# Kernel tuning notes

Hardware: AMD Instinct MI355X
Metric: run time of the kernel (lower is better)

The kernel has to match this reference:

```python
import jax, jax.numpy as jnp
import numpy as np

B, P, D = 16384, 4096, 256

def setup_inputs() -> dict:
    key = jax.random.key(0)
    kx, kp = jax.random.split(key)
    x = jax.random.normal(kx, (B, D), dtype=jnp.float32)
    prototypes = jax.random.normal(kp, (P, D), dtype=jnp.float32)
    return {"x": x, "prototypes": prototypes}

def reference(x, prototypes):
    # Pairwise L2 distance: ||x - p||_2 for every (batch, prototype) pair.
    # GEMM reformulation avoids the O(B*P*D) broadcast intermediate:
    x_sq = jnp.sum(x * x, axis=-1, keepdims=True)                 # [B, 1]
    p_sq = jnp.sum(prototypes * prototypes, axis=-1)[None, :]     # [1, P]
    xp = jnp.einsum('bd,pd->bp', x, prototypes)                   # [B, P]
    sq_dist = jnp.maximum(x_sq + p_sq - 2.0 * xp, 0.0)
    return jnp.sqrt(sq_dist)                                      # [B, P]
```

## Files before the change

### kernel.cpp

```cpp
#include <hip/hip_runtime.h>
#include <hip/hip_bf16.h>

#define B_DIM 16384
#define P_DIM 4096
#define D_DIM 256

typedef float f32x4 __attribute__((ext_vector_type(4)));
typedef __bf16 bf16x8 __attribute__((ext_vector_type(8)));

__device__ __forceinline__ unsigned short f2bf_rne(float f) {
  unsigned int u = __builtin_bit_cast(unsigned int, f);
  u += 0x7fffu + ((u >> 16) & 1u);
  return (unsigned short)(u >> 16);
}

__global__ __launch_bounds__(256) void prep_kernel(
    const float* __restrict__ x, const float* __restrict__ p,
    unsigned short* __restrict__ xb, unsigned short* __restrict__ pb,
    float* __restrict__ xsq, float* __restrict__ psq) {
  int row  = blockIdx.x * 4 + (threadIdx.x >> 6);
  int lane = threadIdx.x & 63;
  const float4* src;
  unsigned short* dst;
  float* sq;
  if (row < B_DIM) {
    src = (const float4*)(x + (size_t)row * D_DIM);
    dst = xb + (size_t)row * D_DIM;
    sq  = xsq + row;
  } else {
    int r = row - B_DIM;
    src = (const float4*)(p + (size_t)r * D_DIM);
    dst = pb + (size_t)r * D_DIM;
    sq  = psq + r;
  }
  float4 v = src[lane];
  ushort4 o;
  o.x = f2bf_rne(v.x); o.y = f2bf_rne(v.y);
  o.z = f2bf_rne(v.z); o.w = f2bf_rne(v.w);
  ((ushort4*)dst)[lane] = o;
  float s = v.x * v.x + v.y * v.y + v.z * v.z + v.w * v.w;
  #pragma unroll
  for (int off = 32; off > 0; off >>= 1) s += __shfl_down(s, off);
  if (lane == 0) *sq = s;
}

__device__ __forceinline__ void async16(const unsigned short* g, void* l) {
  __builtin_amdgcn_global_load_lds(
      (const __attribute__((address_space(1))) void*)g,
      (__attribute__((address_space(3))) void*)l,
      16, 0, 0);
}

__global__ __launch_bounds__(256, 2) void dist_gemm(
    const unsigned short* __restrict__ A,
    const unsigned short* __restrict__ Bm,
    const float* __restrict__ xsq, const float* __restrict__ psq,
    float* __restrict__ out) {
  __shared__ __align__(16) __bf16 As[128 * 32];
  __shared__ __align__(16) __bf16 Bs[128 * 32];

  const int tid  = threadIdx.x;
  const int w    = tid >> 6;
  const int lane = tid & 63;

  const int bid = blockIdx.x;
  const int swz = (bid & 7) * 512 + (bid >> 3);
  const int bm  = swz >> 5;
  const int bn  = swz & 31;

  const int wr = w >> 1;
  const int wc = w & 1;

  f32x4 acc[4][4];
  #pragma unroll
  for (int m = 0; m < 4; ++m)
    #pragma unroll
    for (int n = 0; n < 4; ++n) acc[m][n] = 0.0f;

  const int ofs0 = w * 2048 + lane * 16;
  const int ofs1 = ofs0 + 1024;
  const int r0 = ofs0 >> 6, c0 = (ofs0 & 63) >> 1;
  const int r1 = ofs1 >> 6, c1 = (ofs1 & 63) >> 1;

  const unsigned short* a0 = A  + (size_t)(bm * 128 + r0) * D_DIM + c0;
  const unsigned short* a1 = A  + (size_t)(bm * 128 + r1) * D_DIM + c1;
  const unsigned short* b0 = Bm + (size_t)(bn * 128 + r0) * D_DIM + c0;
  const unsigned short* b1 = Bm + (size_t)(bn * 128 + r1) * D_DIM + c1;

  char* ldsA = (char*)As + w * 2048;
  char* ldsB = (char*)Bs + w * 2048;

  const int ar = wr * 64 + (lane & 15);
  const int br = wc * 64 + (lane & 15);
  const int kk = (lane >> 4) * 8;

  #pragma unroll 1
  for (int kt = 0; kt < D_DIM; kt += 32) {
    async16(a0 + kt, ldsA);
    async16(a1 + kt, ldsA + 1024);
    async16(b0 + kt, ldsB);
    async16(b1 + kt, ldsB + 1024);
    __syncthreads();

    bf16x8 av[4], bv[4];
    #pragma unroll
    for (int m = 0; m < 4; ++m)
      av[m] = *(const bf16x8*)(As + (ar + m * 16) * 32 + kk);
    #pragma unroll
    for (int n = 0; n < 4; ++n)
      bv[n] = *(const bf16x8*)(Bs + (br + n * 16) * 32 + kk);

    #pragma unroll
    for (int m = 0; m < 4; ++m)
      #pragma unroll
      for (int n = 0; n < 4; ++n)
        acc[m][n] = __builtin_amdgcn_mfma_f32_16x16x32_bf16(av[m], bv[n], acc[m][n], 0, 0, 0);
    __syncthreads();
  }

  const int row0 = bm * 128 + wr * 64 + (lane >> 4) * 4;
  const int col0 = bn * 128 + wc * 64 + (lane & 15);
  #pragma unroll
  for (int m = 0; m < 4; ++m) {
    #pragma unroll
    for (int n = 0; n < 4; ++n) {
      const int col = col0 + n * 16;
      const float ps = psq[col];
      #pragma unroll
      for (int j = 0; j < 4; ++j) {
        const int row = row0 + m * 16 + j;
        const float xs = xsq[row];
        float v = fmaf(-2.0f, acc[m][n][j], xs + ps);
        v = fmaxf(v, 0.0f);
        out[(size_t)row * P_DIM + col] = __builtin_sqrtf(v);
      }
    }
  }
}

extern "C" void kernel_launch(void* const* d_in, const int* in_sizes, int n_in,
                              void* d_out, int out_size, void* d_ws, size_t ws_size,
                              hipStream_t stream) {
  const float* x = (const float*)d_in[0];
  const float* p = (const float*)d_in[1];
  float* out = (float*)d_out;

  char* ws = (char*)d_ws;
  unsigned short* xb = (unsigned short*)ws;
  unsigned short* pb = (unsigned short*)(ws + (size_t)B_DIM * D_DIM * 2);
  float* xsq = (float*)(ws + (size_t)(B_DIM + P_DIM) * D_DIM * 2);
  float* psq = xsq + B_DIM;

  prep_kernel<<<(B_DIM + P_DIM) / 4, 256, 0, stream>>>(x, p, xb, pb, xsq, psq);

  dist_gemm<<<(B_DIM / 128) * (P_DIM / 128), 256, 0, stream>>>(xb, pb, xsq, psq, out);
}
```

Measured before the change: 89.35 us.

## Double-buffer LDS with BK=64, XOR-swizzled layout and nontemporal output stores

Raises the K tile from 32 to 64 and double-buffers the LDS tiles, so the async global-to-LDS loads for the next tile overlap the MFMA work on the current one and each tile needs only one barrier. The LDS layout gets an XOR swizzle on the row index to cut bank conflicts on the bf16x8 fragment reads. Output stores become nontemporal to avoid polluting the cache with the large result. LDS use grows to 64KB per block, which may limit occupancy against the launch-bounds target of 2 blocks per CU.

```diff
diff --git a/kernel.cpp b/kernel.cpp
--- a/kernel.cpp
+++ b/kernel.cpp
@@ -4,6 +4,8 @@
 #define B_DIM 16384
 #define P_DIM 4096
 #define D_DIM 256
+#define BK 64
+#define NT (D_DIM / BK)
 
 typedef float f32x4 __attribute__((ext_vector_type(4)));
 typedef __bf16 bf16x8 __attribute__((ext_vector_type(8)));
@@ -56,8 +58,7 @@
     const unsigned short* __restrict__ Bm,
     const float* __restrict__ xsq, const float* __restrict__ psq,
     float* __restrict__ out) {
-  __shared__ __align__(16) __bf16 As[128 * 32];
-  __shared__ __align__(16) __bf16 Bs[128 * 32];
+  __shared__ __align__(16) char lds[2][2][128 * BK * 2];
 
   const int tid  = threadIdx.x;
   const int w    = tid >> 6;
@@ -77,45 +78,67 @@
     #pragma unroll
     for (int n = 0; n < 4; ++n) acc[m][n] = 0.0f;
 
-  const int ofs0 = w * 2048 + lane * 16;
-  const int ofs1 = ofs0 + 1024;
-  const int r0 = ofs0 >> 6, c0 = (ofs0 & 63) >> 1;
-  const int r1 = ofs1 >> 6, c1 = (ofs1 & 63) >> 1;
+  const unsigned short* asrc[4];
+  const unsigned short* bsrc[4];
+  int lofs[4];
+  #pragma unroll
+  for (int l = 0; l < 4; ++l) {
+    int q  = w * 4096 + l * 1024 + lane * 16;
+    int r  = q >> 7;
+    int cb = (q & 127) ^ ((r & 7) << 4);
+    asrc[l] = A  + (size_t)(bm * 128 + r) * D_DIM + (cb >> 1);
+    bsrc[l] = Bm + (size_t)(bn * 128 + r) * D_DIM + (cb >> 1);
+    lofs[l] = w * 4096 + l * 1024;
+  }
 
-  const unsigned short* a0 = A  + (size_t)(bm * 128 + r0) * D_DIM + c0;
-  const unsigned short* a1 = A  + (size_t)(bm * 128 + r1) * D_DIM + c1;
-  const unsigned short* b0 = Bm + (size_t)(bn * 128 + r0) * D_DIM + c0;
-  const unsigned short* b1 = Bm + (size_t)(bn * 128 + r1) * D_DIM + c1;
+#define STAGE(buf, kt) do {                                      \
+    _Pragma("unroll")                                            \
+    for (int l = 0; l < 4; ++l) {                                \
+      async16(asrc[l] + (kt), (void*)(lds[buf][0] + lofs[l]));   \
+      async16(bsrc[l] + (kt), (void*)(lds[buf][1] + lofs[l]));   \
+    } } while (0)
 
-  char* ldsA = (char*)As + w * 2048;
-  char* ldsB = (char*)Bs + w * 2048;
+  const int ar   = wr * 64 + (lane & 15);
+  const int br   = wc * 64 + (lane & 15);
+  const int xr   = (lane & 7) << 4;
+  const int kcol = (lane >> 4) * 16;
 
-  const int ar = wr * 64 + (lane & 15);
-  const int br = wc * 64 + (lane & 15);
-  const int kk = (lane >> 4) * 8;
+  STAGE(0, 0);
+  asm volatile("s_waitcnt vmcnt(0)" ::: "memory");
+  __builtin_amdgcn_s_barrier();
+  __builtin_amdgcn_sched_barrier(0);
 
-  #pragma unroll 1
-  for (int kt = 0; kt < D_DIM; kt += 32) {
-    async16(a0 + kt, ldsA);
-    async16(a1 + kt, ldsA + 1024);
-    async16(b0 + kt, ldsB);
-    async16(b1 + kt, ldsB + 1024);
-    __syncthreads();
+  #pragma unroll
+  for (int t = 0; t < NT; ++t) {
+    if (t < NT - 1) STAGE((t + 1) & 1, (t + 1) * BK);
 
-    bf16x8 av[4], bv[4];
+    const char* La = lds[t & 1][0];
+    const char* Lb = lds[t & 1][1];
     #pragma unroll
-    for (int m = 0; m < 4; ++m)
-      av[m] = *(const bf16x8*)(As + (ar + m * 16) * 32 + kk);
-    #pragma unroll
-    for (int n = 0; n < 4; ++n)
-      bv[n] = *(const bf16x8*)(Bs + (br + n * 16) * 32 + kk);
+    for (int qk = 0; qk < 2; ++qk) {
+      bf16x8 av[4], bv[4];
+      #pragma unroll
+      for (int m = 0; m < 4; ++m) {
+        int row = ar + m * 16;
+        av[m] = *(const bf16x8*)(La + row * 128 + ((kcol + qk * 64) ^ xr));
+      }
+      #pragma unroll
+      for (int n = 0; n < 4; ++n) {
+        int row = br + n * 16;
+        bv[n] = *(const bf16x8*)(Lb + row * 128 + ((kcol + qk * 64) ^ xr));
+      }
+      #pragma unroll
+      for (int m = 0; m < 4; ++m)
+        #pragma unroll
+        for (int n = 0; n < 4; ++n)
+          acc[m][n] = __builtin_amdgcn_mfma_f32_16x16x32_bf16(av[m], bv[n], acc[m][n], 0, 0, 0);
+    }
 
-    #pragma unroll
-    for (int m = 0; m < 4; ++m)
-      #pragma unroll
-      for (int n = 0; n < 4; ++n)
-        acc[m][n] = __builtin_amdgcn_mfma_f32_16x16x32_bf16(av[m], bv[n], acc[m][n], 0, 0, 0);
-    __syncthreads();
+    if (t < NT - 1) {
+      asm volatile("s_waitcnt vmcnt(0)" ::: "memory");
+      __builtin_amdgcn_s_barrier();
+      __builtin_amdgcn_sched_barrier(0);
+    }
   }
 
   const int row0 = bm * 128 + wr * 64 + (lane >> 4) * 4;
@@ -132,10 +155,12 @@
         const float xs = xsq[row];
         float v = fmaf(-2.0f, acc[m][n][j], xs + ps);
         v = fmaxf(v, 0.0f);
-        out[(size_t)row * P_DIM + col] = __builtin_sqrtf(v);
+        __builtin_nontemporal_store(__builtin_sqrtf(v),
+                                    &out[(size_t)row * P_DIM + col]);
       }
     }
   }
+#undef STAGE
 }
 
 extern "C" void kernel_launch(void* const* d_in, const int* in_sizes, int n_in,
```

Result: slower. 92.72 us (+3.8%).

## Pre-swizzle bf16 operands into MFMA fragment layout and drop LDS staging

Applied to the files above, without the earlier changes.

The prep kernel now writes x and prototypes in bf16 using a blocked layout that matches the MFMA 16x16x32 fragment order. The GEMM can then have each wave load its operand fragments straight from global memory with coalesced 16-byte loads, which removes the LDS copies and the __syncthreads barriers. The block tiling changes to a 64-row A tile shared by four waves, each covering a different 64-column group. The launch bound rises to 3 blocks per CU, and the grid is mapped by XCD so neighbouring blocks reuse A in L2. The cost is that the four waves do not share their B fragments, so there is no reuse through LDS and more data comes from L2.

```diff
diff --git a/kernel.cpp b/kernel.cpp
--- a/kernel.cpp
+++ b/kernel.cpp
@@ -18,58 +18,61 @@
     const float* __restrict__ x, const float* __restrict__ p,
     unsigned short* __restrict__ xb, unsigned short* __restrict__ pb,
     float* __restrict__ xsq, float* __restrict__ psq) {
-  int row  = blockIdx.x * 4 + (threadIdx.x >> 6);
-  int lane = threadIdx.x & 63;
-  const float4* src;
+  const int rg = blockIdx.x;
+  const int t = threadIdx.x;
+  const int row = t >> 4;
+  const int kq  = t & 15;
+
+  const float* src;
   unsigned short* dst;
   float* sq;
-  if (row < B_DIM) {
-    src = (const float4*)(x + (size_t)row * D_DIM);
-    dst = xb + (size_t)row * D_DIM;
-    sq  = xsq + row;
+  if (rg < B_DIM / 16) {
+    src = x + (size_t)rg * 16 * D_DIM;
+    dst = xb + (size_t)rg * 4096;
+    sq  = xsq + rg * 16;
   } else {
-    int r = row - B_DIM;
-    src = (const float4*)(p + (size_t)r * D_DIM);
-    dst = pb + (size_t)r * D_DIM;
-    sq  = psq + r;
+    const int r = rg - B_DIM / 16;
+    src = p + (size_t)r * 16 * D_DIM;
+    dst = pb + (size_t)r * 4096;
+    sq  = psq + r * 16;
   }
-  float4 v = src[lane];
-  ushort4 o;
-  o.x = f2bf_rne(v.x); o.y = f2bf_rne(v.y);
-  o.z = f2bf_rne(v.z); o.w = f2bf_rne(v.w);
-  ((ushort4*)dst)[lane] = o;
-  float s = v.x * v.x + v.y * v.y + v.z * v.z + v.w * v.w;
+
+  float s = 0.0f;
   #pragma unroll
-  for (int off = 32; off > 0; off >>= 1) s += __shfl_down(s, off);
-  if (lane == 0) *sq = s;
+  for (int pass = 0; pass < 4; ++pass) {
+    float4 v = *(const float4*)(src + row * D_DIM + pass * 64 + kq * 4);
+    s += v.x * v.x + v.y * v.y + v.z * v.z + v.w * v.w;
+    ushort4 o;
+    o.x = f2bf_rne(v.x); o.y = f2bf_rne(v.y);
+    o.z = f2bf_rne(v.z); o.w = f2bf_rne(v.w);
+    const int kc = pass * 8 + (kq >> 1);
+    *(ushort4*)(dst + kc * 128 + row * 8 + (kq & 1) * 4) = o;
+  }
+  s += __shfl_xor(s, 1);
+  s += __shfl_xor(s, 2);
+  s += __shfl_xor(s, 4);
+  s += __shfl_xor(s, 8);
+  if (kq == 0) sq[row] = s;
 }
 
-__device__ __forceinline__ void async16(const unsigned short* g, void* l) {
-  __builtin_amdgcn_global_load_lds(
-      (const __attribute__((address_space(1))) void*)g,
-      (__attribute__((address_space(3))) void*)l,
-      16, 0, 0);
-}
-
-__global__ __launch_bounds__(256, 2) void dist_gemm(
-    const unsigned short* __restrict__ A,
-    const unsigned short* __restrict__ Bm,
+__global__ __launch_bounds__(256, 3) void dist_gemm(
+    const unsigned short* __restrict__ A2,
+    const unsigned short* __restrict__ B2,
     const float* __restrict__ xsq, const float* __restrict__ psq,
     float* __restrict__ out) {
-  __shared__ __align__(16) __bf16 As[128 * 32];
-  __shared__ __align__(16) __bf16 Bs[128 * 32];
-
   const int tid  = threadIdx.x;
   const int w    = tid >> 6;
   const int lane = tid & 63;
+  const int bid  = blockIdx.x;
 
-  const int bid = blockIdx.x;
-  const int swz = (bid & 7) * 512 + (bid >> 3);
-  const int bm  = swz >> 5;
-  const int bn  = swz & 31;
+  const int xcd = bid & 7;
+  const int idx = bid >> 3;
+  const int am  = idx >> 1;
+  const int bnb = xcd * 2 + (idx & 1);
+  const int bn  = bnb * 4 + w;
 
-  const int wr = w >> 1;
-  const int wc = w & 1;
+  const char* Abase = (const char*)A2 + (size_t)am * 32768 + lane * 16;
+  const char* Bbase = (const char*)B2 + (size_t)bn * 32768 + lane * 16;
 
   f32x4 acc[4][4];
   #pragma unroll
@@ -77,62 +80,41 @@
     #pragma unroll
     for (int n = 0; n < 4; ++n) acc[m][n] = 0.0f;
 
-  const int ofs0 = w * 2048 + lane * 16;
-  const int ofs1 = ofs0 + 1024;
-  const int r0 = ofs0 >> 6, c0 = (ofs0 & 63) >> 1;
-  const int r1 = ofs1 >> 6, c1 = (ofs1 & 63) >> 1;
-
-  const unsigned short* a0 = A  + (size_t)(bm * 128 + r0) * D_DIM + c0;
-  const unsigned short* a1 = A  + (size_t)(bm * 128 + r1) * D_DIM + c1;
-  const unsigned short* b0 = Bm + (size_t)(bn * 128 + r0) * D_DIM + c0;
-  const unsigned short* b1 = Bm + (size_t)(bn * 128 + r1) * D_DIM + c1;
-
-  char* ldsA = (char*)As + w * 2048;
-  char* ldsB = (char*)Bs + w * 2048;
-
-  const int ar = wr * 64 + (lane & 15);
-  const int br = wc * 64 + (lane & 15);
-  const int kk = (lane >> 4) * 8;
-
-  #pragma unroll 1
-  for (int kt = 0; kt < D_DIM; kt += 32) {
-    async16(a0 + kt, ldsA);
-    async16(a1 + kt, ldsA + 1024);
-    async16(b0 + kt, ldsB);
-    async16(b1 + kt, ldsB + 1024);
-    __syncthreads();
-
+  #pragma unroll
+  for (int kt = 0; kt < 8; ++kt) {
     bf16x8 av[4], bv[4];
     #pragma unroll
     for (int m = 0; m < 4; ++m)
-      av[m] = *(const bf16x8*)(As + (ar + m * 16) * 32 + kk);
+      av[m] = *(const bf16x8*)(Abase + m * 8192 + kt * 1024);
     #pragma unroll
     for (int n = 0; n < 4; ++n)
-      bv[n] = *(const bf16x8*)(Bs + (br + n * 16) * 32 + kk);
-
+      bv[n] = *(const bf16x8*)(Bbase + n * 8192 + kt * 1024);
     #pragma unroll
     for (int m = 0; m < 4; ++m)
       #pragma unroll
       for (int n = 0; n < 4; ++n)
         acc[m][n] = __builtin_amdgcn_mfma_f32_16x16x32_bf16(av[m], bv[n], acc[m][n], 0, 0, 0);
-    __syncthreads();
   }
 
-  const int row0 = bm * 128 + wr * 64 + (lane >> 4) * 4;
-  const int col0 = bn * 128 + wc * 64 + (lane & 15);
+  const int rowb = am * 64 + ((lane >> 4) << 2);
+  const int colb = bn * 64 + (lane & 15);
+  f32x4 xs4[4];
+  #pragma unroll
+  for (int m = 0; m < 4; ++m)
+    xs4[m] = *(const f32x4*)(xsq + rowb + m * 16);
+  float psv[4];
+  #pragma unroll
+  for (int n = 0; n < 4; ++n) psv[n] = psq[colb + n * 16];
+
   #pragma unroll
   for (int m = 0; m < 4; ++m) {
     #pragma unroll
-    for (int n = 0; n < 4; ++n) {
-      const int col = col0 + n * 16;
-      const float ps = psq[col];
+    for (int j = 0; j < 4; ++j) {
+      float* orow = out + (size_t)(rowb + m * 16 + j) * P_DIM + colb;
       #pragma unroll
-      for (int j = 0; j < 4; ++j) {
-        const int row = row0 + m * 16 + j;
-        const float xs = xsq[row];
-        float v = fmaf(-2.0f, acc[m][n][j], xs + ps);
-        v = fmaxf(v, 0.0f);
-        out[(size_t)row * P_DIM + col] = __builtin_sqrtf(v);
+      for (int n = 0; n < 4; ++n) {
+        float v = fmaf(-2.0f, acc[m][n][j], xs4[m][j] + psv[n]);
+        orow[n * 16] = __builtin_sqrtf(fmaxf(v, 0.0f));
       }
     }
   }
@@ -151,7 +133,7 @@
   float* xsq = (float*)(ws + (size_t)(B_DIM + P_DIM) * D_DIM * 2);
   float* psq = xsq + B_DIM;
 
-  prep_kernel<<<(B_DIM + P_DIM) / 4, 256, 0, stream>>>(x, p, xb, pb, xsq, psq);
+  prep_kernel<<<(B_DIM + P_DIM) / 16, 256, 0, stream>>>(x, p, xb, pb, xsq, psq);
 
-  dist_gemm<<<(B_DIM / 128) * (P_DIM / 128), 256, 0, stream>>>(xb, pb, xsq, psq, out);
+  dist_gemm<<<4096, 256, 0, stream>>>(xb, pb, xsq, psq, out);
 }
```

New measurement: 104.5 us. 17.0% more time.

## Triple-buffer LDS pipeline with swizzled layout and vectorized epilogue stores

Applied to the files above, without the earlier changes.

Replaces the single-buffer load/sync/compute loop with a three-stage LDS ring fed by async global-to-LDS loads, using vmcnt waits and one barrier per step so the next tiles' loads overlap the MFMA work. The LDS layout is XOR-swizzled to reduce bank conflicts on fragment reads, and the MFMA operands are swapped so each lane holds four consecutive output columns. That lets the epilogue write float4 stores, cutting store instruction count, and raises the occupancy hint to 3 blocks per CU. The cost is more LDS per block and hand-tuned waitcnt logic that depends on how the compiler schedules the loads.

```diff
diff --git a/kernel.cpp b/kernel.cpp
--- a/kernel.cpp
+++ b/kernel.cpp
@@ -4,6 +4,8 @@
 #define B_DIM 16384
 #define P_DIM 4096
 #define D_DIM 256
+#define BK 32
+#define NSTEP (D_DIM / BK)
 
 typedef float f32x4 __attribute__((ext_vector_type(4)));
 typedef __bf16 bf16x8 __attribute__((ext_vector_type(8)));
@@ -44,26 +46,25 @@
   if (lane == 0) *sq = s;
 }
 
-__device__ __forceinline__ void async16(const unsigned short* g, void* l) {
+__device__ __forceinline__ void async16(const unsigned short* g, const void* l) {
   __builtin_amdgcn_global_load_lds(
       (const __attribute__((address_space(1))) void*)g,
       (__attribute__((address_space(3))) void*)l,
       16, 0, 0);
 }
 
-__global__ __launch_bounds__(256, 2) void dist_gemm(
+__global__ __launch_bounds__(256, 3) void dist_gemm(
     const unsigned short* __restrict__ A,
     const unsigned short* __restrict__ Bm,
     const float* __restrict__ xsq, const float* __restrict__ psq,
     float* __restrict__ out) {
-  __shared__ __align__(16) __bf16 As[128 * 32];
-  __shared__ __align__(16) __bf16 Bs[128 * 32];
+  __shared__ __align__(16) char lds[3][2][8192];
 
   const int tid  = threadIdx.x;
   const int w    = tid >> 6;
   const int lane = tid & 63;
+  const int bid  = blockIdx.x;
 
-  const int bid = blockIdx.x;
   const int swz = (bid & 7) * 512 + (bid >> 3);
   const int bm  = swz >> 5;
   const int bn  = swz & 31;
@@ -71,71 +72,87 @@
   const int wr = w >> 1;
   const int wc = w & 1;
 
+  const int trow = tid >> 2;
+  const int tcol = (((tid & 3) ^ (trow & 3)) << 3);
+  const unsigned short* aSrc = A  + (size_t)(bm * 128 + trow) * D_DIM + tcol;
+  const unsigned short* bSrc = Bm + (size_t)(bn * 128 + trow) * D_DIM + tcol;
+  const int ldst = tid * 16;
+
+#define STAGE(bufi, ktE) do { _Pragma("unroll")                                \
+    for (int i = 0; i < 2; ++i) {                                              \
+      async16(aSrc + (size_t)i * 64 * D_DIM + (ktE),                           \
+              (const void*)(&lds[bufi][0][0] + i * 4096 + ldst));              \
+      async16(bSrc + (size_t)i * 64 * D_DIM + (ktE),                           \
+              (const void*)(&lds[bufi][1][0] + i * 4096 + ldst));              \
+    } } while (0)
+
+  const int arow = wr * 64 + (lane & 15);
+  const int brow = wc * 64 + (lane & 15);
+  const int koff = (((lane >> 4) ^ (lane & 3)) << 4);
+
   f32x4 acc[4][4];
   #pragma unroll
   for (int m = 0; m < 4; ++m)
     #pragma unroll
     for (int n = 0; n < 4; ++n) acc[m][n] = 0.0f;
 
-  const int ofs0 = w * 2048 + lane * 16;
-  const int ofs1 = ofs0 + 1024;
-  const int r0 = ofs0 >> 6, c0 = (ofs0 & 63) >> 1;
-  const int r1 = ofs1 >> 6, c1 = (ofs1 & 63) >> 1;
+  STAGE(0, 0);
+  STAGE(1, BK);
 
-  const unsigned short* a0 = A  + (size_t)(bm * 128 + r0) * D_DIM + c0;
-  const unsigned short* a1 = A  + (size_t)(bm * 128 + r1) * D_DIM + c1;
-  const unsigned short* b0 = Bm + (size_t)(bn * 128 + r0) * D_DIM + c0;
-  const unsigned short* b1 = Bm + (size_t)(bn * 128 + r1) * D_DIM + c1;
+  #pragma unroll
+  for (int t = 0; t < NSTEP; ++t) {
+    if (t < NSTEP - 1) asm volatile("s_waitcnt vmcnt(4)" ::: "memory");
+    else               asm volatile("s_waitcnt vmcnt(0)" ::: "memory");
+    __builtin_amdgcn_s_barrier();
+    __builtin_amdgcn_sched_barrier(0);
 
-  char* ldsA = (char*)As + w * 2048;
-  char* ldsB = (char*)Bs + w * 2048;
+    if (t < NSTEP - 2) {
+      const int nb = (t + 2) % 3;
+      STAGE(nb, (t + 2) * BK);
+    }
 
-  const int ar = wr * 64 + (lane & 15);
-  const int br = wc * 64 + (lane & 15);
-  const int kk = (lane >> 4) * 8;
-
-  #pragma unroll 1
-  for (int kt = 0; kt < D_DIM; kt += 32) {
-    async16(a0 + kt, ldsA);
-    async16(a1 + kt, ldsA + 1024);
-    async16(b0 + kt, ldsB);
-    async16(b1 + kt, ldsB + 1024);
-    __syncthreads();
-
+    const char* La = &lds[t % 3][0][0];
+    const char* Lb = &lds[t % 3][1][0];
     bf16x8 av[4], bv[4];
     #pragma unroll
     for (int m = 0; m < 4; ++m)
-      av[m] = *(const bf16x8*)(As + (ar + m * 16) * 32 + kk);
+      av[m] = *(const bf16x8*)(La + (arow + m * 16) * 64 + koff);
     #pragma unroll
     for (int n = 0; n < 4; ++n)
-      bv[n] = *(const bf16x8*)(Bs + (br + n * 16) * 32 + kk);
-
+      bv[n] = *(const bf16x8*)(Lb + (brow + n * 16) * 64 + koff);
     #pragma unroll
     for (int m = 0; m < 4; ++m)
       #pragma unroll
       for (int n = 0; n < 4; ++n)
-        acc[m][n] = __builtin_amdgcn_mfma_f32_16x16x32_bf16(av[m], bv[n], acc[m][n], 0, 0, 0);
-    __syncthreads();
+        acc[m][n] = __builtin_amdgcn_mfma_f32_16x16x32_bf16(bv[n], av[m], acc[m][n], 0, 0, 0);
   }
 
-  const int row0 = bm * 128 + wr * 64 + (lane >> 4) * 4;
-  const int col0 = bn * 128 + wc * 64 + (lane & 15);
+  const int xrowB = bm * 128 + wr * 64;
+  const int pcolB = bn * 128 + wc * 64;
+  const int rL = lane & 15;
+  const int hL = lane >> 4;
+
+  f32x4 ps[4];
+  #pragma unroll
+  for (int n = 0; n < 4; ++n)
+    ps[n] = *(const f32x4*)(psq + pcolB + n * 16 + hL * 4);
+
   #pragma unroll
   for (int m = 0; m < 4; ++m) {
+    const float xs = xsq[xrowB + m * 16 + rL];
+    float* orow = out + (size_t)(xrowB + m * 16 + rL) * P_DIM + pcolB + hL * 4;
     #pragma unroll
     for (int n = 0; n < 4; ++n) {
-      const int col = col0 + n * 16;
-      const float ps = psq[col];
+      f32x4 v;
       #pragma unroll
       for (int j = 0; j < 4; ++j) {
-        const int row = row0 + m * 16 + j;
-        const float xs = xsq[row];
-        float v = fmaf(-2.0f, acc[m][n][j], xs + ps);
-        v = fmaxf(v, 0.0f);
-        out[(size_t)row * P_DIM + col] = __builtin_sqrtf(v);
+        float d = fmaf(-2.0f, acc[m][n][j], xs + ps[n][j]);
+        v[j] = __builtin_sqrtf(fmaxf(d, 0.0f));
       }
+      *(f32x4*)(orow + n * 16) = v;
     }
   }
+#undef STAGE
 }
 
 extern "C" void kernel_launch(void* const* d_in, const int* in_sizes, int n_in,
```

Measured after the change: 92.47 us. 3.5% more time.
